# Kernel optimization log

Hardware: AMD Instinct MI355X
Metric: run time of the kernel (lower is better)

Reference implementation:

```python
import jax, jax.numpy as jnp
import numpy as np

B, S, IN_F, OUT_F = 4, 2048, 4096, 4096

def setup_inputs() -> dict:
    key = jax.random.key(0)
    k1, k2, k3 = jax.random.split(key, 3)
    # int8 activations and weights (symmetric range)
    x = jax.random.randint(k1, (B, S, IN_F), -128, 128, dtype=jnp.int32).astype(jnp.int8)
    weight_q = jax.random.randint(k2, (OUT_F, IN_F), -128, 128, dtype=jnp.int32).astype(jnp.int8)
    scale_x = jnp.float32(0.05)   # activation quant scale
    scale_w = jnp.float32(0.02)   # weight quant scale (scalar, per-tensor)
    scale_y = jax.random.uniform(k3, (OUT_F,), minval=0.5, maxval=2.0, dtype=jnp.float32)  # per-output-row scale
    return {"x": x, "weight_q": weight_q, "scale_x": scale_x, "scale_w": scale_w, "scale_y": scale_y}

def reference(x, weight_q, scale_x, scale_w, scale_y):
    # int8 GEMM with int32 accumulation: [B,S,IN] @ [OUT,IN]^T -> [B,S,OUT]
    acc = jax.lax.dot_general(x, weight_q, ((((2,), (1,)), ((), ()))),
                              preferred_element_type=jnp.int32)
    # fused requantization scale: scale_x * scale_w / scale_y  -> [OUT]
    requant_scale = (scale_x * scale_w / scale_y).astype(jnp.float32)
    out_f = acc.astype(jnp.float32) * requant_scale  # broadcast over last dim
    out_q = jnp.clip(jnp.round(out_f), -128, 127).astype(jnp.int8)
    return out_q, scale_y
```

## Files before the change

### kernel.cpp

```cpp
#include <hip/hip_runtime.h>
#include <cstdint>


#define MDIM 8192
#define NDIM 4096
#define KDIM 4096
#define BM 256
#define BN 256
#define BKB 128
#define NT (KDIM / BKB)
#define KTILES (KDIM / BKB)

typedef int v4i __attribute__((ext_vector_type(4)));

#define FENCE() asm volatile("" ::: "memory")
#define BAR()                     \
  do {                            \
    FENCE();                      \
    __builtin_amdgcn_s_barrier(); \
    FENCE();                      \
  } while (0)

__device__ __forceinline__ uint32_t pack4(int a, int b, int c, int d) {
  return (uint32_t)(a & 0xFF) | ((uint32_t)(b & 0xFF) << 8) |
         ((uint32_t)(c & 0xFF) << 16) | ((uint32_t)(d & 0xFF) << 24);
}

__global__ __launch_bounds__(256) void pack_kernel(
    const int* __restrict__ x32, const int* __restrict__ w32,
    const float* __restrict__ sy, uint8_t* __restrict__ x8f,
    uint8_t* __restrict__ w8f, float* __restrict__ tail) {
  const int t = blockIdx.x * 256 + threadIdx.x;
  if (t < NDIM) tail[t] = sy[t];
  const int NXC = (MDIM / 16) * KDIM;
  const int NWC = (NDIM / 16) * KDIM;
  if (t >= NXC + NWC) return;
  const int* src;
  uint8_t* dst;
  int chunk;
  if (t < NXC) {
    chunk = t;
    src = x32;
    dst = x8f;
  } else {
    chunk = t - NXC;
    src = w32;
    dst = w8f;
  }
  const int blk = chunk >> 11;
  const int cb = chunk & 2047;
  const int mb = blk >> 5;
  const int kt = blk & 31;
  const int region = cb >> 6;
  const int lpos = cb & 63;
  const int rf = region >> 1, kh = region & 1;
  const int kl = lpos >> 4, fr = lpos & 15;
  const int r = mb * 256 + rf * 16 + fr;
  const int k0 = kt * 128 + kh * 64 + kl * 16;
  const int* s = src + (size_t)r * KDIM + k0;
  v4i a0 = *(const v4i*)(s + 0);
  v4i a1 = *(const v4i*)(s + 4);
  v4i a2 = *(const v4i*)(s + 8);
  v4i a3 = *(const v4i*)(s + 12);
  v4i o;
  o[0] = (int)pack4(a0[0], a0[1], a0[2], a0[3]);
  o[1] = (int)pack4(a1[0], a1[1], a1[2], a1[3]);
  o[2] = (int)pack4(a2[0], a2[1], a2[2], a2[3]);
  o[3] = (int)pack4(a3[0], a3[1], a3[2], a3[3]);
  *(v4i*)(dst + (size_t)chunk * 16) = o;
}

__global__ __launch_bounds__(512, 2) void gemm_kernel(
    const uint8_t* __restrict__ A8, const uint8_t* __restrict__ B8,
    const float* __restrict__ sxp, const float* __restrict__ swp,
    const float* __restrict__ syp, float* __restrict__ out) {
  __shared__ __align__(16) uint8_t lds[131072];

  const int tid = threadIdx.x;
  const int lane = tid & 63;
  const int wave = tid >> 6;

  const int wg = ((int)blockIdx.x % 8) * 64 + (int)blockIdx.x / 8;
  const int mb = wg >> 4;
  const int nb = wg & 15;

  const int wm2 = wave >> 2;
  const int wn4 = wave & 3;

  const uint8_t* Abase = A8 + ((size_t)(mb * KTILES) << 15);
  const uint8_t* Bbase = B8 + ((size_t)(nb * KTILES) << 15);

  v4i acc[8][4];
#pragma unroll
  for (int i = 0; i < 8; i++)
#pragma unroll
    for (int j = 0; j < 4; j++) acc[i][j] = (v4i){0, 0, 0, 0};

  const uint32_t sdst = (uint32_t)tid * 16;

  auto stage = [&](int t) {
    const uint32_t lb = (uint32_t)(t & 1) * 65536u;
    const uint8_t* as = Abase + ((size_t)t << 15) + sdst;
    const uint8_t* bs = Bbase + ((size_t)t << 15) + sdst;
#pragma unroll
    for (int r = 0; r < 4; ++r) {
      __builtin_amdgcn_global_load_lds(
          (const __attribute__((address_space(1))) void*)(as + r * 8192),
          (__attribute__((address_space(3))) void*)(lds + lb + r * 8192 + sdst),
          16, 0, 0);
      __builtin_amdgcn_global_load_lds(
          (const __attribute__((address_space(1))) void*)(bs + r * 8192),
          (__attribute__((address_space(3))) void*)(lds + lb + 32768 + r * 8192 +
                                                    sdst),
          16, 0, 0);
    }
  };

  stage(0);

  for (int t = 0; t < NT; ++t) {
    if (t + 1 < NT) {
      stage(t + 1);
      asm volatile("s_waitcnt vmcnt(8)" ::: "memory");
    } else {
      asm volatile("s_waitcnt vmcnt(0)" ::: "memory");
    }
    BAR();

    const uint8_t* La = lds + (uint32_t)(t & 1) * 65536u;
    const uint8_t* Lb = La + 32768;
#pragma unroll
    for (int kh = 0; kh < 2; ++kh) {
      v4i af[8], bf[4];
#pragma unroll
      for (int i = 0; i < 8; i++)
        af[i] = *(const v4i*)(La + ((((wm2 * 8 + i) << 1) + kh) << 10) +
                              lane * 16);
#pragma unroll
      for (int j = 0; j < 4; j++)
        bf[j] = *(const v4i*)(Lb + ((((wn4 * 4 + j) << 1) + kh) << 10) +
                              lane * 16);
#pragma unroll
      for (int i = 0; i < 8; i++)
#pragma unroll
        for (int j = 0; j < 4; j++)
          acc[i][j] = __builtin_amdgcn_mfma_i32_16x16x64_i8(af[i], bf[j],
                                                            acc[i][j], 0, 0, 0);
    }
    BAR();
  }

  const float s = sxp[0] * swp[0];
  const int kl = lane >> 4;
  const int fr = lane & 15;
  const int wrow = mb * 256 + wm2 * 128;
  const int wcol = nb * 256 + wn4 * 64;
#pragma unroll
  for (int j = 0; j < 4; j++) {
    const int col = wcol + j * 16 + fr;
    const float rs = s / syp[col];
#pragma unroll
    for (int i = 0; i < 8; i++) {
      const int row0 = wrow + i * 16 + kl * 4;
#pragma unroll
      for (int r = 0; r < 4; r++) {
        float v = rintf((float)acc[i][j][r] * rs);
        v = fminf(127.f, fmaxf(-128.f, v));
        out[(size_t)(row0 + r) * NDIM + col] = v;
      }
    }
  }
}

extern "C" void kernel_launch(void* const* d_in, const int* in_sizes, int n_in,
                              void* d_out, int out_size, void* d_ws, size_t ws_size,
                              hipStream_t stream) {
  const int* x32 = (const int*)d_in[0];
  const int* w32 = (const int*)d_in[1];
  const float* sx = (const float*)d_in[2];
  const float* sw = (const float*)d_in[3];
  const float* sy = (const float*)d_in[4];
  float* out = (float*)d_out;
  float* tail = out + (size_t)MDIM * NDIM;

  uint8_t* x8f = (uint8_t*)d_ws;
  uint8_t* w8f = x8f + (size_t)MDIM * KDIM;

  const int total = (MDIM / 16) * KDIM + (NDIM / 16) * KDIM;
  pack_kernel<<<total / 256, 256, 0, stream>>>(x32, w32, sy, x8f, w8f, tail);

  const int nblocks = (MDIM / BM) * (NDIM / BN);
  gemm_kernel<<<nblocks, 512, 0, stream>>>(x8f, w8f, sx, sw, sy, out);
}
```

Measured before the change: 182.2 us.

## Interleave k-half tile loads with MFMA phases using finer-grained staging and setprio

Changes the packed layout so each 128-wide k-tile is split into two contiguous k-halves. The main loop now runs four compute phases per tile, each loading a subset of fragments from LDS and issuing part of the next tile's global-to-LDS copy. MFMA blocks are wrapped in s_setprio, and waitcnts are placed so loads for the next tile overlap with compute, a ping-pong style schedule. The cost is more barriers per tile and tighter ordering assumptions on vmcnt.

Measured after the change: 186.1 us. 2.2% more time.

```diff
diff --git a/kernel.cpp b/kernel.cpp
--- a/kernel.cpp
+++ b/kernel.cpp
@@ -9,7 +9,6 @@
 #define BN 256
 #define BKB 128
 #define NT (KDIM / BKB)
-#define KTILES (KDIM / BKB)
 
 typedef int v4i __attribute__((ext_vector_type(4)));
 
@@ -53,7 +52,7 @@
   const int kt = blk & 31;
   const int region = cb >> 6;
   const int lpos = cb & 63;
-  const int rf = region >> 1, kh = region & 1;
+  const int kh = region >> 4, rf = region & 15;
   const int kl = lpos >> 4, fr = lpos & 15;
   const int r = mb * 256 + rf * 16 + fr;
   const int k0 = kt * 128 + kh * 64 + kl * 16;
@@ -87,8 +86,13 @@
   const int wm2 = wave >> 2;
   const int wn4 = wave & 3;
 
-  const uint8_t* Abase = A8 + ((size_t)(mb * KTILES) << 15);
-  const uint8_t* Bbase = B8 + ((size_t)(nb * KTILES) << 15);
+  const uint8_t* Abase = A8 + ((size_t)(mb * 32) << 15);
+  const uint8_t* Bbase = B8 + ((size_t)(nb * 32) << 15);
+
+  const uint32_t sdst = (uint32_t)tid * 16;
+  const uint32_t lane16 = (uint32_t)lane * 16;
+  const uint32_t aoff = (uint32_t)(wm2 * 8) << 10;
+  const uint32_t boff = (uint32_t)(wn4 * 4) << 10;
 
   v4i acc[8][4];
 #pragma unroll
@@ -96,57 +100,108 @@
 #pragma unroll
     for (int j = 0; j < 4; j++) acc[i][j] = (v4i){0, 0, 0, 0};
 
-  const uint32_t sdst = (uint32_t)tid * 16;
-
-  auto stage = [&](int t) {
-    const uint32_t lb = (uint32_t)(t & 1) * 65536u;
-    const uint8_t* as = Abase + ((size_t)t << 15) + sdst;
-    const uint8_t* bs = Bbase + ((size_t)t << 15) + sdst;
-#pragma unroll
-    for (int r = 0; r < 4; ++r) {
-      __builtin_amdgcn_global_load_lds(
-          (const __attribute__((address_space(1))) void*)(as + r * 8192),
-          (__attribute__((address_space(3))) void*)(lds + lb + r * 8192 + sdst),
-          16, 0, 0);
-      __builtin_amdgcn_global_load_lds(
-          (const __attribute__((address_space(1))) void*)(bs + r * 8192),
-          (__attribute__((address_space(3))) void*)(lds + lb + 32768 + r * 8192 +
-                                                    sdst),
-          16, 0, 0);
-    }
+  auto gload = [&](const uint8_t* src, uint32_t ldsoff) {
+    __builtin_amdgcn_global_load_lds(
+        (const __attribute__((address_space(1))) void*)src,
+        (__attribute__((address_space(3))) void*)(lds + ldsoff), 16, 0, 0);
   };
-
-  stage(0);
+  auto stageA = [&](int t, int kh) {
+    const uint32_t lb = (uint32_t)(t & 1) * 65536u + (uint32_t)kh * 16384u + sdst;
+    const uint8_t* s = Abase + ((size_t)t << 15) + (uint32_t)(kh * 16384) + sdst;
+    gload(s, lb);
+    gload(s + 8192, lb + 8192);
+  };
+  auto stageB = [&](int t, int kh) {
+    const uint32_t lb =
+        (uint32_t)(t & 1) * 65536u + 32768u + (uint32_t)kh * 16384u + sdst;
+    const uint8_t* s = Bbase + ((size_t)t << 15) + (uint32_t)(kh * 16384) + sdst;
+    gload(s, lb);
+    gload(s + 8192, lb + 8192);
+  };
+
+  stageA(0, 0);
+  stageB(0, 0);
+  stageA(0, 1);
+  stageB(0, 1);
+  asm volatile("s_waitcnt vmcnt(4)" ::: "memory");
+  BAR();
 
   for (int t = 0; t < NT; ++t) {
-    if (t + 1 < NT) {
-      stage(t + 1);
-      asm volatile("s_waitcnt vmcnt(8)" ::: "memory");
-    } else {
+    const uint8_t* LA = lds + (uint32_t)(t & 1) * 65536u;
+    const uint8_t* LB = LA + 32768u;
+    const bool pre = (t + 1 < NT);
+    v4i af[4], bf[4];
+
+#pragma unroll
+    for (int i = 0; i < 4; i++)
+      af[i] = *(const v4i*)(LA + aoff + (i << 10) + lane16);
+#pragma unroll
+    for (int j = 0; j < 4; j++)
+      bf[j] = *(const v4i*)(LB + boff + (j << 10) + lane16);
+    if (pre) stageA(t + 1, 0);
+    BAR();
+    __builtin_amdgcn_s_setprio(1);
+#pragma unroll
+    for (int i = 0; i < 4; i++)
+#pragma unroll
+      for (int j = 0; j < 4; j++)
+        acc[i][j] =
+            __builtin_amdgcn_mfma_i32_16x16x64_i8(af[i], bf[j], acc[i][j], 0, 0, 0);
+    __builtin_amdgcn_s_setprio(0);
+    BAR();
+
+#pragma unroll
+    for (int i = 0; i < 4; i++)
+      af[i] = *(const v4i*)(LA + aoff + ((4 + i) << 10) + lane16);
+    if (pre) stageB(t + 1, 0);
+    BAR();
+    __builtin_amdgcn_s_setprio(1);
+#pragma unroll
+    for (int i = 0; i < 4; i++)
+#pragma unroll
+      for (int j = 0; j < 4; j++)
+        acc[4 + i][j] =
+            __builtin_amdgcn_mfma_i32_16x16x64_i8(af[i], bf[j], acc[4 + i][j], 0, 0, 0);
+    __builtin_amdgcn_s_setprio(0);
+    if (pre)
+      asm volatile("s_waitcnt vmcnt(4)" ::: "memory");
+    else
       asm volatile("s_waitcnt vmcnt(0)" ::: "memory");
-    }
-    BAR();
-
-    const uint8_t* La = lds + (uint32_t)(t & 1) * 65536u;
-    const uint8_t* Lb = La + 32768;
-#pragma unroll
-    for (int kh = 0; kh < 2; ++kh) {
-      v4i af[8], bf[4];
-#pragma unroll
-      for (int i = 0; i < 8; i++)
-        af[i] = *(const v4i*)(La + ((((wm2 * 8 + i) << 1) + kh) << 10) +
-                              lane * 16);
-#pragma unroll
-      for (int j = 0; j < 4; j++)
-        bf[j] = *(const v4i*)(Lb + ((((wn4 * 4 + j) << 1) + kh) << 10) +
-                              lane * 16);
-#pragma unroll
-      for (int i = 0; i < 8; i++)
-#pragma unroll
-        for (int j = 0; j < 4; j++)
-          acc[i][j] = __builtin_amdgcn_mfma_i32_16x16x64_i8(af[i], bf[j],
-                                                            acc[i][j], 0, 0, 0);
-    }
+    BAR();
+
+#pragma unroll
+    for (int i = 0; i < 4; i++)
+      af[i] = *(const v4i*)(LA + 16384u + aoff + (i << 10) + lane16);
+#pragma unroll
+    for (int j = 0; j < 4; j++)
+      bf[j] = *(const v4i*)(LB + 16384u + boff + (j << 10) + lane16);
+    if (pre) stageA(t + 1, 1);
+    BAR();
+    __builtin_amdgcn_s_setprio(1);
+#pragma unroll
+    for (int i = 0; i < 4; i++)
+#pragma unroll
+      for (int j = 0; j < 4; j++)
+        acc[i][j] =
+            __builtin_amdgcn_mfma_i32_16x16x64_i8(af[i], bf[j], acc[i][j], 0, 0, 0);
+    __builtin_amdgcn_s_setprio(0);
+    BAR();
+
+#pragma unroll
+    for (int i = 0; i < 4; i++)
+      af[i] = *(const v4i*)(LA + 16384u + aoff + ((4 + i) << 10) + lane16);
+    if (pre) stageB(t + 1, 1);
+    BAR();
+    __builtin_amdgcn_s_setprio(1);
+#pragma unroll
+    for (int i = 0; i < 4; i++)
+#pragma unroll
+      for (int j = 0; j < 4; j++)
+        acc[4 + i][j] =
+            __builtin_amdgcn_mfma_i32_16x16x64_i8(af[i], bf[j], acc[4 + i][j], 0, 0, 0);
+    __builtin_amdgcn_s_setprio(0);
+    if (pre)
+      asm volatile("s_waitcnt vmcnt(4)" ::: "memory");
     BAR();
   }
 
```

## Restructure GEMM K-loop to one barrier per tile with k-half-major packed layout

Applied to the files above, without the earlier changes.

The packed operand layout now stores both k-halves as contiguous 16KB regions instead of interleaving them per row fragment. The main loop waits for all outstanding loads, takes a single barrier, and only then issues the next tile's global-to-LDS loads, which removes the second barrier per iteration. All 24 fragment reads are hoisted ahead of both MFMA batches. The trade-off is that the next tile's prefetch no longer overlaps the wait on the current tile, and holding all fragments at once raises register pressure.

Measured after the change: 185.8 us. No clear change (+2.0%).

```diff
diff --git a/kernel.cpp b/kernel.cpp
--- a/kernel.cpp
+++ b/kernel.cpp
@@ -9,7 +9,6 @@
 #define BN 256
 #define BKB 128
 #define NT (KDIM / BKB)
-#define KTILES (KDIM / BKB)
 
 typedef int v4i __attribute__((ext_vector_type(4)));
 
@@ -53,7 +52,7 @@
   const int kt = blk & 31;
   const int region = cb >> 6;
   const int lpos = cb & 63;
-  const int rf = region >> 1, kh = region & 1;
+  const int kh = region >> 4, rf = region & 15;
   const int kl = lpos >> 4, fr = lpos & 15;
   const int r = mb * 256 + rf * 16 + fr;
   const int k0 = kt * 128 + kh * 64 + kl * 16;
@@ -87,8 +86,13 @@
   const int wm2 = wave >> 2;
   const int wn4 = wave & 3;
 
-  const uint8_t* Abase = A8 + ((size_t)(mb * KTILES) << 15);
-  const uint8_t* Bbase = B8 + ((size_t)(nb * KTILES) << 15);
+  const uint8_t* Abase = A8 + ((size_t)(mb * 32) << 15);
+  const uint8_t* Bbase = B8 + ((size_t)(nb * 32) << 15);
+
+  const uint32_t sdst = (uint32_t)tid * 16;
+  const uint32_t lane16 = (uint32_t)lane * 16;
+  const uint32_t aoff = (uint32_t)(wm2 * 8) << 10;
+  const uint32_t boff = (uint32_t)(wn4 * 4) << 10;
 
   v4i acc[8][4];
 #pragma unroll
@@ -96,58 +100,58 @@
 #pragma unroll
     for (int j = 0; j < 4; j++) acc[i][j] = (v4i){0, 0, 0, 0};
 
-  const uint32_t sdst = (uint32_t)tid * 16;
-
+  auto gload = [&](const uint8_t* src, uint32_t ldsoff) {
+    __builtin_amdgcn_global_load_lds(
+        (const __attribute__((address_space(1))) void*)src,
+        (__attribute__((address_space(3))) void*)(lds + ldsoff), 16, 0, 0);
+  };
   auto stage = [&](int t) {
-    const uint32_t lb = (uint32_t)(t & 1) * 65536u;
-    const uint8_t* as = Abase + ((size_t)t << 15) + sdst;
-    const uint8_t* bs = Bbase + ((size_t)t << 15) + sdst;
+    const uint32_t lb = (uint32_t)(t & 1) * 65536u + sdst;
+    const uint8_t* sa = Abase + ((size_t)t << 15) + sdst;
+    const uint8_t* sb = Bbase + ((size_t)t << 15) + sdst;
 #pragma unroll
     for (int r = 0; r < 4; ++r) {
-      __builtin_amdgcn_global_load_lds(
-          (const __attribute__((address_space(1))) void*)(as + r * 8192),
-          (__attribute__((address_space(3))) void*)(lds + lb + r * 8192 + sdst),
-          16, 0, 0);
-      __builtin_amdgcn_global_load_lds(
-          (const __attribute__((address_space(1))) void*)(bs + r * 8192),
-          (__attribute__((address_space(3))) void*)(lds + lb + 32768 + r * 8192 +
-                                                    sdst),
-          16, 0, 0);
+      gload(sa + r * 8192, lb + r * 8192);
+      gload(sb + r * 8192, lb + 32768u + r * 8192);
     }
   };
 
   stage(0);
 
   for (int t = 0; t < NT; ++t) {
-    if (t + 1 < NT) {
-      stage(t + 1);
-      asm volatile("s_waitcnt vmcnt(8)" ::: "memory");
-    } else {
-      asm volatile("s_waitcnt vmcnt(0)" ::: "memory");
-    }
+    asm volatile("s_waitcnt vmcnt(0)" ::: "memory");
     BAR();
+    if (t + 1 < NT) stage(t + 1);
 
-    const uint8_t* La = lds + (uint32_t)(t & 1) * 65536u;
-    const uint8_t* Lb = La + 32768;
+    const uint8_t* LA = lds + (uint32_t)(t & 1) * 65536u;
+    const uint8_t* LB = LA + 32768u;
+
+    v4i af0[8], bf0[4], af1[8], bf1[4];
 #pragma unroll
-    for (int kh = 0; kh < 2; ++kh) {
-      v4i af[8], bf[4];
+    for (int j = 0; j < 4; j++)
+      bf0[j] = *(const v4i*)(LB + boff + (j << 10) + lane16);
 #pragma unroll
-      for (int i = 0; i < 8; i++)
-        af[i] = *(const v4i*)(La + ((((wm2 * 8 + i) << 1) + kh) << 10) +
-                              lane * 16);
+    for (int i = 0; i < 8; i++)
+      af0[i] = *(const v4i*)(LA + aoff + (i << 10) + lane16);
+#pragma unroll
+    for (int j = 0; j < 4; j++)
+      bf1[j] = *(const v4i*)(LB + 16384u + boff + (j << 10) + lane16);
+#pragma unroll
+    for (int i = 0; i < 8; i++)
+      af1[i] = *(const v4i*)(LA + 16384u + aoff + (i << 10) + lane16);
+
+#pragma unroll
+    for (int i = 0; i < 8; i++)
 #pragma unroll
       for (int j = 0; j < 4; j++)
-        bf[j] = *(const v4i*)(Lb + ((((wn4 * 4 + j) << 1) + kh) << 10) +
-                              lane * 16);
+        acc[i][j] =
+            __builtin_amdgcn_mfma_i32_16x16x64_i8(af0[i], bf0[j], acc[i][j], 0, 0, 0);
 #pragma unroll
-      for (int i = 0; i < 8; i++)
+    for (int i = 0; i < 8; i++)
 #pragma unroll
-        for (int j = 0; j < 4; j++)
-          acc[i][j] = __builtin_amdgcn_mfma_i32_16x16x64_i8(af[i], bf[j],
-                                                            acc[i][j], 0, 0, 0);
-    }
-    BAR();
+      for (int j = 0; j < 4; j++)
+        acc[i][j] =
+            __builtin_amdgcn_mfma_i32_16x16x64_i8(af1[i], bf1[j], acc[i][j], 0, 0, 0);
   }
 
   const float s = sxp[0] * swp[0];
```
